# Kernel optimization log

Measured on AMD Instinct MI355X. Metric: run time of the kernel, lower is better.

The kernel has to match this reference:

```python
import jax, jax.numpy as jnp
import numpy as np

NUM_HEADS = 16
DIM_HEAD = 64
SCALE = DIM_HEAD ** -0.5


def setup_inputs() -> dict:
    key = jax.random.key(0)
    k1, k2, k3 = jax.random.split(key, 3)
    b, s, h = 2, 2048, 1024
    x = jax.random.normal(k1, (b, s, h), dtype=jnp.float32)
    w_qkv = jax.random.normal(k2, (3 * h, h), dtype=jnp.float32) * (h ** -0.5)
    w_out = jax.random.normal(k3, (h, h), dtype=jnp.float32) * (h ** -0.5)
    b_out = jnp.zeros((h,), dtype=jnp.float32)
    return {"x": x, "w_qkv": w_qkv, "w_out": w_out, "b_out": b_out}


def reference(x, w_qkv, w_out, b_out):
    b, s, hid = x.shape
    # qkv projection (no bias): [b, s, 3*hid]
    qkv = jnp.einsum('bsh,oh->bso', x, w_qkv)
    # split order in original rearrange is (qkv, heads, dim_head)
    qkv = qkv.reshape(b, s, 3, NUM_HEADS, DIM_HEAD)
    q = jnp.transpose(qkv[:, :, 0], (0, 2, 1, 3))  # [b, H, s, d]
    k = jnp.transpose(qkv[:, :, 1], (0, 2, 1, 3))
    v = jnp.transpose(qkv[:, :, 2], (0, 2, 1, 3))
    # naive attention: full [b, H, s, s] score matrix, as in the source
    att = jnp.einsum('bhxd,bhyd->bhxy', q, k) * SCALE
    att = jax.nn.softmax(att, axis=-1)
    out = jnp.einsum('bhxy,bhyd->bhxd', att, v)  # [b, H, s, d]
    out = jnp.transpose(out, (0, 2, 1, 3)).reshape(b, s, NUM_HEADS * DIM_HEAD)
    return jnp.einsum('bsi,oi->bso', out, w_out) + b_out
```

## Files before the change

### kernel.cpp

```cpp
#include <hip/hip_runtime.h>
#include <hip/hip_bf16.h>

#define B_ 2
#define S_ 2048
#define HID 1024
#define NH 16
#define DH 64
#define QKV_N (3*HID)
#define M_ROWS (B_*S_)

typedef __attribute__((ext_vector_type(8))) short short8;
typedef __attribute__((ext_vector_type(4))) short short4v;
typedef __attribute__((ext_vector_type(4))) float floatx4;
typedef unsigned int uint;

__device__ __forceinline__ short8 load8(const __hip_bfloat16* p) {
    return *(const short8*)p;
}

#if __has_builtin(__builtin_amdgcn_exp2f)
#define EXP2F(x) __builtin_amdgcn_exp2f(x)
#else
#define EXP2F(x) exp2f(x)
#endif

__device__ __forceinline__ uint pack_bf16_2(float lo, float hi) {
    uint ul = __float_as_uint(lo) + 0x8000u;
    uint uh = __float_as_uint(hi) + 0x8000u;
    return __builtin_amdgcn_perm(uh, ul, 0x07060302);
}
__device__ __forceinline__ uint pack_bf16_2_rtne(float lo, float hi) {
    uint ul = __float_as_uint(lo); ul += 0x7FFFu + ((ul >> 16) & 1u);
    uint uh = __float_as_uint(hi); uh += 0x7FFFu + ((uh >> 16) & 1u);
    return __builtin_amdgcn_perm(uh, ul, 0x07060302);
}

#define ASYNC16(gptr, lptr) \
    __builtin_amdgcn_global_load_lds((const __attribute__((address_space(1))) void*)(gptr), \
                                     (__attribute__((address_space(3))) void*)(lptr), 16, 0, 0)

__global__ __launch_bounds__(256) void cvt_all(
    const float* __restrict__ x, const float* __restrict__ wq,
    const float* __restrict__ wo, __hip_bfloat16* __restrict__ out)
{
    const int n0 = M_ROWS * HID, n1 = QKV_N * HID;
    int i = (blockIdx.x * 256 + threadIdx.x) * 4;
    const float* src; int off;
    if (i < n0)           { src = x;  off = i; }
    else if (i < n0 + n1) { src = wq; off = i - n0; }
    else                  { src = wo; off = i - n0 - n1; }
    float4 v = *(const float4*)(src + off);
    uint2 r;
    r.x = pack_bf16_2_rtne(v.x, v.y);
    r.y = pack_bf16_2_rtne(v.z, v.w);
    *(uint2*)(out + i) = r;
}

#define BK 64
template<int MODE>
__global__ __launch_bounds__(256) void gemm_bt_kernel(
    const __hip_bfloat16* __restrict__ A,
    const __hip_bfloat16* __restrict__ Bw,
    const float* __restrict__ biasf,
    __hip_bfloat16* __restrict__ C,
    float* __restrict__ Cf,
    __hip_bfloat16* __restrict__ VT,
    int Mdim, int Ndim, int Kdim)
{
    __shared__ alignas(16) __hip_bfloat16 As[2][128 * BK];
    __shared__ alignas(16) __hip_bfloat16 Bs[2][128 * BK];

    const int tid  = threadIdx.x;
    const int wave = tid >> 6;
    const int lane = tid & 63;
    const int q = lane >> 4;
    const int r = lane & 15;
    const int m_blk = blockIdx.y * 128;
    const int n_blk = blockIdx.x * 128;
    const int wm = (wave >> 1) * 64;
    const int wn = (wave & 1) * 64;

    const int srow = tid >> 3;
    const int cglob = (tid & 7) ^ ((tid >> 3) & 7);
    const __hip_bfloat16* gA = A + (size_t)(m_blk + srow) * Kdim + cglob * 8;
    const __hip_bfloat16* gB = Bw + (size_t)(n_blk + srow) * Kdim + cglob * 8;
    const int ldso = tid * 8;

    floatx4 acc[4][4];
#pragma unroll
    for (int i = 0; i < 4; i++)
#pragma unroll
        for (int j = 0; j < 4; j++) acc[i][j] = (floatx4){0.f, 0.f, 0.f, 0.f};

    const int niter = Kdim / BK;
#pragma unroll
    for (int c = 0; c < 4; c++) {
        ASYNC16(gA + (size_t)(c * 32) * Kdim, &As[0][ldso + c * 2048]);
        ASYNC16(gB + (size_t)(c * 32) * Kdim, &Bs[0][ldso + c * 2048]);
    }
    __builtin_amdgcn_s_waitcnt(0x0F70);
    __syncthreads();

    for (int it = 0; it < niter; it++) {
        const int cur = it & 1, nxt = cur ^ 1;
        if (it + 1 < niter) {
            const int kt = (it + 1) * BK;
#pragma unroll
            for (int c = 0; c < 4; c++) {
                ASYNC16(gA + kt + (size_t)(c * 32) * Kdim, &As[nxt][ldso + c * 2048]);
                ASYNC16(gB + kt + (size_t)(c * 32) * Kdim, &Bs[nxt][ldso + c * 2048]);
            }
        }
#pragma unroll
        for (int kh = 0; kh < 2; kh++) {
            short8 a[4], b[4];
#pragma unroll
            for (int i = 0; i < 4; i++)
                a[i] = *(const short8*)&As[cur][(wm + i * 16 + r) * BK + (((kh * 4 + q) ^ (r & 7)) * 8)];
#pragma unroll
            for (int j = 0; j < 4; j++)
                b[j] = *(const short8*)&Bs[cur][(wn + j * 16 + r) * BK + (((kh * 4 + q) ^ (r & 7)) * 8)];
#pragma unroll
            for (int i = 0; i < 4; i++)
#pragma unroll
                for (int j = 0; j < 4; j++)
                    acc[i][j] = __builtin_amdgcn_mfma_f32_16x16x32_bf16(a[i], b[j], acc[i][j], 0, 0, 0);
        }
        __builtin_amdgcn_s_waitcnt(0x0F70);
        __syncthreads();
    }

#pragma unroll
    for (int i = 0; i < 4; i++) {
#pragma unroll
        for (int j = 0; j < 4; j++) {
#pragma unroll
            for (int reg = 0; reg < 4; reg++) {
                int m = m_blk + wm + i * 16 + q * 4 + reg;
                int n = n_blk + wn + j * 16 + r;
                float v = acc[i][j][reg];
                if (MODE == 2) {
                    Cf[(size_t)m * Ndim + n] = v + biasf[n];
                } else {
                    __hip_bfloat16 hv = __float2bfloat16(v);
                    if (n < 2 * HID) {
                        C[(size_t)m * QKV_N + n] = hv;
                    } else {
                        int dfull = n - 2 * HID;
                        int bidx = m >> 11;
                        int s = m & (S_ - 1);
                        int c = s & 63;
                        int sp = (s & ~63) | ((c & 15) << 2) | ((c >> 4) & 3);
                        VT[((size_t)bidx * HID + dfull) * S_ + sp] = hv;
                    }
                }
            }
        }
    }
}

#define KT 64
#define PPAD 72
#define SCALE2 0.18033688f
#define FM2 23.083120f

__global__ __launch_bounds__(256, 2) void flash_kernel(
    const __hip_bfloat16* __restrict__ qkv,
    const __hip_bfloat16* __restrict__ VTp,
    __hip_bfloat16* __restrict__ O)
{
    __shared__ alignas(16) __hip_bfloat16 lds_k[2][64 * 64];
    __shared__ alignas(16) __hip_bfloat16 lds_v[2][64 * 64];
    __shared__ alignas(16) __hip_bfloat16 lds_p[4][32 * PPAD];

    const int tid  = threadIdx.x;
    const int wave = tid >> 6;
    const int lane = tid & 63;
    const int q = lane >> 4;
    const int r = lane & 15;
    const int bh = blockIdx.x;
    const int b  = bh >> 4;
    const int h  = bh & 15;
    const int s0 = blockIdx.y * 128 + wave * 32;

    const __hip_bfloat16* Qbase = qkv + (size_t)b * S_ * QKV_N + h * DH;
    const __hip_bfloat16* Kbase = Qbase + HID;
    const __hip_bfloat16* Vbase = VTp + ((size_t)b * HID + h * DH) * S_;

    const int sr = wave * 16 + (lane >> 3);
    const int cglob = (lane & 7) ^ ((lane >> 3) & 7);
    const __hip_bfloat16* gK = Kbase + (size_t)sr * QKV_N + cglob * 8;
    const __hip_bfloat16* gV = Vbase + (size_t)sr * S_ + cglob * 8;
    const int ldso = sr * 64 + (lane & 7) * 8;

    short8 a_q[2][2];
#pragma unroll
    for (int rt = 0; rt < 2; rt++)
#pragma unroll
        for (int kh = 0; kh < 2; kh++)
            a_q[rt][kh] = load8(Qbase + (size_t)(s0 + rt * 16 + r) * QKV_N + kh * 32 + q * 8);

    floatx4 o_acc[2][4];
    floatx4 l_acc[2];
#pragma unroll
    for (int rt = 0; rt < 2; rt++) {
        l_acc[rt] = (floatx4){0.f, 0.f, 0.f, 0.f};
#pragma unroll
        for (int nb = 0; nb < 4; nb++) o_acc[rt][nb] = (floatx4){0.f, 0.f, 0.f, 0.f};
    }

    short8 ones;
#pragma unroll
    for (int i = 0; i < 8; i++) ones[i] = (short)0x3F80;

    __hip_bfloat16* Pw = &lds_p[wave][0];

#pragma unroll
    for (int c = 0; c < 2; c++) {
        ASYNC16(gK + (size_t)(c * 8) * QKV_N, &lds_k[0][ldso + c * 512]);
        ASYNC16(gV + (size_t)(c * 8) * S_,    &lds_v[0][ldso + c * 512]);
    }
    __builtin_amdgcn_s_waitcnt(0x0F70);
    __syncthreads();

    for (int it = 0; it < S_ / KT; it++) {
        const int cur = it & 1, nxt = cur ^ 1;
        if (it + 1 < S_ / KT) {
            const int ktn = (it + 1) * KT;
#pragma unroll
            for (int c = 0; c < 2; c++) {
                ASYNC16(gK + (size_t)(ktn + c * 8) * QKV_N, &lds_k[nxt][ldso + c * 512]);
                ASYNC16(gV + (size_t)(c * 8) * S_ + ktn,    &lds_v[nxt][ldso + c * 512]);
            }
        }

        short8 bk[4][2];
#pragma unroll
        for (int ct = 0; ct < 4; ct++)
#pragma unroll
            for (int kh = 0; kh < 2; kh++)
                bk[ct][kh] = *(const short8*)&lds_k[cur][(ct * 16 + r) * 64 + ((kh * 4 + q) ^ (r & 7)) * 8];

#pragma unroll
        for (int rt = 0; rt < 2; rt++) {
            floatx4 sc[4];
#pragma unroll
            for (int ct = 0; ct < 4; ct++) {
                floatx4 z = (floatx4){0.f, 0.f, 0.f, 0.f};
                z = __builtin_amdgcn_mfma_f32_16x16x32_bf16(a_q[rt][0], bk[ct][0], z, 0, 0, 0);
                z = __builtin_amdgcn_mfma_f32_16x16x32_bf16(a_q[rt][1], bk[ct][1], z, 0, 0, 0);
                sc[ct] = z;
            }
#pragma unroll
            for (int reg = 0; reg < 4; reg++) {
                float e0 = EXP2F(fmaf(sc[0][reg], SCALE2, -FM2));
                float e1 = EXP2F(fmaf(sc[1][reg], SCALE2, -FM2));
                float e2 = EXP2F(fmaf(sc[2][reg], SCALE2, -FM2));
                float e3 = EXP2F(fmaf(sc[3][reg], SCALE2, -FM2));
                uint2 pw;
                pw.x = pack_bf16_2(e0, e1);
                pw.y = pack_bf16_2(e2, e3);
                *(uint2*)&Pw[(rt * 16 + q * 4 + reg) * PPAD + 4 * r] = pw;
            }
        }
        __builtin_amdgcn_s_waitcnt(0xc07f);

        short8 vb[4][2];
#pragma unroll
        for (int nb = 0; nb < 4; nb++)
#pragma unroll
            for (int kh = 0; kh < 2; kh++)
                vb[nb][kh] = *(const short8*)&lds_v[cur][(nb * 16 + r) * 64 + ((kh * 4 + q) ^ (r & 7)) * 8];

#pragma unroll
        for (int rt = 0; rt < 2; rt++) {
            short8 pa0 = *(const short8*)&Pw[(rt * 16 + r) * PPAD + q * 8];
            short8 pa1 = *(const short8*)&Pw[(rt * 16 + r) * PPAD + 32 + q * 8];
            l_acc[rt] = __builtin_amdgcn_mfma_f32_16x16x32_bf16(pa0, ones, l_acc[rt], 0, 0, 0);
            l_acc[rt] = __builtin_amdgcn_mfma_f32_16x16x32_bf16(pa1, ones, l_acc[rt], 0, 0, 0);
#pragma unroll
            for (int nb = 0; nb < 4; nb++) {
                o_acc[rt][nb] = __builtin_amdgcn_mfma_f32_16x16x32_bf16(pa0, vb[nb][0], o_acc[rt][nb], 0, 0, 0);
                o_acc[rt][nb] = __builtin_amdgcn_mfma_f32_16x16x32_bf16(pa1, vb[nb][1], o_acc[rt][nb], 0, 0, 0);
            }
        }
        __builtin_amdgcn_s_waitcnt(0x0F70);
        __syncthreads();
    }

#pragma unroll
    for (int rt = 0; rt < 2; rt++) {
#pragma unroll
        for (int reg = 0; reg < 4; reg++) {
            float inv = 1.f / l_acc[rt][reg];
            int srow2 = s0 + rt * 16 + q * 4 + reg;
            __hip_bfloat16* Orow = O + ((size_t)b * S_ + srow2) * HID + h * DH;
#pragma unroll
            for (int nb = 0; nb < 4; nb++)
                Orow[nb * 16 + r] = __float2bfloat16(o_acc[rt][nb][reg] * inv);
        }
    }
}

extern "C" void kernel_launch(void* const* d_in, const int* in_sizes, int n_in,
                              void* d_out, int out_size, void* d_ws, size_t ws_size,
                              hipStream_t stream) {
    const float* x_f     = (const float*)d_in[0];
    const float* w_qkv_f = (const float*)d_in[1];
    const float* w_out_f = (const float*)d_in[2];
    const float* b_out_f = (const float*)d_in[3];
    float* out = (float*)d_out;

    __hip_bfloat16* xb      = (__hip_bfloat16*)d_ws;
    __hip_bfloat16* wqkvb   = xb    + (size_t)M_ROWS * HID;
    __hip_bfloat16* woutb   = wqkvb + (size_t)QKV_N * HID;
    __hip_bfloat16* qkv_ws  = woutb + (size_t)HID * HID;
    __hip_bfloat16* vt_ws   = qkv_ws + (size_t)M_ROWS * QKV_N;
    __hip_bfloat16* attn_ws = vt_ws + (size_t)B_ * HID * S_;

    dim3 blk(256);
    {
        int ntot = M_ROWS * HID + QKV_N * HID + HID * HID;
        cvt_all<<<dim3(ntot / 1024), blk, 0, stream>>>(x_f, w_qkv_f, w_out_f, xb);
    }

    gemm_bt_kernel<1><<<dim3(QKV_N / 128, M_ROWS / 128), blk, 0, stream>>>(
        xb, wqkvb, nullptr, qkv_ws, nullptr, vt_ws, M_ROWS, QKV_N, HID);
    flash_kernel<<<dim3(B_ * NH, S_ / 128), dim3(256), 0, stream>>>(qkv_ws, vt_ws, attn_ws);
    gemm_bt_kernel<2><<<dim3(HID / 128, M_ROWS / 128), blk, 0, stream>>>(
        attn_ws, woutb, b_out_f, nullptr, out, nullptr, M_ROWS, HID, HID);
}
```

Baseline: 203.6 us.

## Triple-buffer GEMM and flash-attention loads with single barrier per iteration

Both the GEMM and flash kernels move from double-buffered async global-to-LDS loads to a three-stage ring buffer. Each iteration now uses a partial vmcnt wait and a raw s_barrier, replacing the full drain plus __syncthreads, so two tiles stay in flight while one is computed. The GEMM also drops to BK=32 with unswizzled LDS layout, gains an M-tile template parameter with occupancy hints, and the output projection uses 64-row tiles to launch more blocks. The costs are more LDS per block and possible bank conflicts from removing the XOR swizzle in the GEMM.

```diff
diff --git a/kernel.cpp b/kernel.cpp
--- a/kernel.cpp
+++ b/kernel.cpp
@@ -38,6 +38,7 @@
 #define ASYNC16(gptr, lptr) \
     __builtin_amdgcn_global_load_lds((const __attribute__((address_space(1))) void*)(gptr), \
                                      (__attribute__((address_space(3))) void*)(lptr), 16, 0, 0)
+#define RAW_BARRIER() asm volatile("s_barrier" ::: "memory")
 
 __global__ __launch_bounds__(256) void cvt_all(
     const float* __restrict__ x, const float* __restrict__ wq,
@@ -56,9 +57,10 @@
     *(uint2*)(out + i) = r;
 }
 
-#define BK 64
-template<int MODE>
-__global__ __launch_bounds__(256) void gemm_bt_kernel(
+#define BK 32
+#define NITER 32
+template<int MODE, int TMB>
+__global__ __launch_bounds__(256, (TMB == 128) ? 3 : 4) void gemm_bt_kernel(
     const __hip_bfloat16* __restrict__ A,
     const __hip_bfloat16* __restrict__ Bw,
     const float* __restrict__ biasf,
@@ -67,71 +69,73 @@
     __hip_bfloat16* __restrict__ VT,
     int Mdim, int Ndim, int Kdim)
 {
-    __shared__ alignas(16) __hip_bfloat16 As[2][128 * BK];
-    __shared__ alignas(16) __hip_bfloat16 Bs[2][128 * BK];
+    constexpr int NI = TMB / 32;
+    constexpr int CA = TMB / 64;
+    constexpr int WAITG = 0x0F70 | (CA + 2);
+    __shared__ alignas(16) __hip_bfloat16 As[3][TMB * BK];
+    __shared__ alignas(16) __hip_bfloat16 Bs[3][128 * BK];
 
     const int tid  = threadIdx.x;
     const int wave = tid >> 6;
     const int lane = tid & 63;
     const int q = lane >> 4;
     const int r = lane & 15;
-    const int m_blk = blockIdx.y * 128;
+    const int m_blk = blockIdx.y * TMB;
     const int n_blk = blockIdx.x * 128;
-    const int wm = (wave >> 1) * 64;
+    const int wm = (wave >> 1) * (TMB / 2);
     const int wn = (wave & 1) * 64;
 
-    const int srow = tid >> 3;
-    const int cglob = (tid & 7) ^ ((tid >> 3) & 7);
-    const __hip_bfloat16* gA = A + (size_t)(m_blk + srow) * Kdim + cglob * 8;
-    const __hip_bfloat16* gB = Bw + (size_t)(n_blk + srow) * Kdim + cglob * 8;
-    const int ldso = tid * 8;
-
-    floatx4 acc[4][4];
-#pragma unroll
-    for (int i = 0; i < 4; i++)
+    const __hip_bfloat16* Abase = A + (size_t)m_blk * Kdim;
+    const __hip_bfloat16* Bbase = Bw + (size_t)n_blk * Kdim;
+
+    floatx4 acc[NI][4];
+#pragma unroll
+    for (int i = 0; i < NI; i++)
 #pragma unroll
         for (int j = 0; j < 4; j++) acc[i][j] = (floatx4){0.f, 0.f, 0.f, 0.f};
 
-    const int niter = Kdim / BK;
-#pragma unroll
-    for (int c = 0; c < 4; c++) {
-        ASYNC16(gA + (size_t)(c * 32) * Kdim, &As[0][ldso + c * 2048]);
-        ASYNC16(gB + (size_t)(c * 32) * Kdim, &Bs[0][ldso + c * 2048]);
-    }
+    auto stage = [&](int bf, int kt) {
+#pragma unroll
+        for (int c = 0; c < CA; c++) {
+            int ch = tid + c * 256;
+            ASYNC16(Abase + (size_t)(ch >> 2) * Kdim + kt + (ch & 3) * 8, &As[bf][ch * 8]);
+        }
+#pragma unroll
+        for (int c = 0; c < 2; c++) {
+            int ch = tid + c * 256;
+            ASYNC16(Bbase + (size_t)(ch >> 2) * Kdim + kt + (ch & 3) * 8, &Bs[bf][ch * 8]);
+        }
+    };
+    auto compute = [&](int bf) {
+        short8 a[NI], b[4];
+#pragma unroll
+        for (int i = 0; i < NI; i++) a[i] = *(const short8*)&As[bf][(wm + i * 16 + r) * BK + q * 8];
+#pragma unroll
+        for (int j = 0; j < 4; j++) b[j] = *(const short8*)&Bs[bf][(wn + j * 16 + r) * BK + q * 8];
+#pragma unroll
+        for (int i = 0; i < NI; i++)
+#pragma unroll
+            for (int j = 0; j < 4; j++)
+                acc[i][j] = __builtin_amdgcn_mfma_f32_16x16x32_bf16(a[i], b[j], acc[i][j], 0, 0, 0);
+    };
+
+    stage(0, 0);
+    stage(1, BK);
+    for (int it = 0; it < NITER - 2; it++) {
+        __builtin_amdgcn_s_waitcnt(WAITG);
+        RAW_BARRIER();
+        stage((it + 2) % 3, (it + 2) * BK);
+        compute(it % 3);
+    }
+    __builtin_amdgcn_s_waitcnt(WAITG);
+    RAW_BARRIER();
+    compute((NITER - 2) % 3);
     __builtin_amdgcn_s_waitcnt(0x0F70);
-    __syncthreads();
-
-    for (int it = 0; it < niter; it++) {
-        const int cur = it & 1, nxt = cur ^ 1;
-        if (it + 1 < niter) {
-            const int kt = (it + 1) * BK;
-#pragma unroll
-            for (int c = 0; c < 4; c++) {
-                ASYNC16(gA + kt + (size_t)(c * 32) * Kdim, &As[nxt][ldso + c * 2048]);
-                ASYNC16(gB + kt + (size_t)(c * 32) * Kdim, &Bs[nxt][ldso + c * 2048]);
-            }
-        }
-#pragma unroll
-        for (int kh = 0; kh < 2; kh++) {
-            short8 a[4], b[4];
-#pragma unroll
-            for (int i = 0; i < 4; i++)
-                a[i] = *(const short8*)&As[cur][(wm + i * 16 + r) * BK + (((kh * 4 + q) ^ (r & 7)) * 8)];
-#pragma unroll
-            for (int j = 0; j < 4; j++)
-                b[j] = *(const short8*)&Bs[cur][(wn + j * 16 + r) * BK + (((kh * 4 + q) ^ (r & 7)) * 8)];
-#pragma unroll
-            for (int i = 0; i < 4; i++)
-#pragma unroll
-                for (int j = 0; j < 4; j++)
-                    acc[i][j] = __builtin_amdgcn_mfma_f32_16x16x32_bf16(a[i], b[j], acc[i][j], 0, 0, 0);
-        }
-        __builtin_amdgcn_s_waitcnt(0x0F70);
-        __syncthreads();
-    }
-
-#pragma unroll
-    for (int i = 0; i < 4; i++) {
+    RAW_BARRIER();
+    compute((NITER - 1) % 3);
+
+#pragma unroll
+    for (int i = 0; i < NI; i++) {
 #pragma unroll
         for (int j = 0; j < 4; j++) {
 #pragma unroll
@@ -169,8 +173,8 @@
     const __hip_bfloat16* __restrict__ VTp,
     __hip_bfloat16* __restrict__ O)
 {
-    __shared__ alignas(16) __hip_bfloat16 lds_k[2][64 * 64];
-    __shared__ alignas(16) __hip_bfloat16 lds_v[2][64 * 64];
+    __shared__ alignas(16) __hip_bfloat16 lds_k[3][64 * 64];
+    __shared__ alignas(16) __hip_bfloat16 lds_v[3][64 * 64];
     __shared__ alignas(16) __hip_bfloat16 lds_p[4][32 * PPAD];
 
     const int tid  = threadIdx.x;
@@ -193,13 +197,6 @@
     const __hip_bfloat16* gV = Vbase + (size_t)sr * S_ + cglob * 8;
     const int ldso = sr * 64 + (lane & 7) * 8;
 
-    short8 a_q[2][2];
-#pragma unroll
-    for (int rt = 0; rt < 2; rt++)
-#pragma unroll
-        for (int kh = 0; kh < 2; kh++)
-            a_q[rt][kh] = load8(Qbase + (size_t)(s0 + rt * 16 + r) * QKV_N + kh * 32 + q * 8);
-
     floatx4 o_acc[2][4];
     floatx4 l_acc[2];
 #pragma unroll
@@ -215,32 +212,22 @@
 
     __hip_bfloat16* Pw = &lds_p[wave][0];
 
-#pragma unroll
-    for (int c = 0; c < 2; c++) {
-        ASYNC16(gK + (size_t)(c * 8) * QKV_N, &lds_k[0][ldso + c * 512]);
-        ASYNC16(gV + (size_t)(c * 8) * S_,    &lds_v[0][ldso + c * 512]);
-    }
-    __builtin_amdgcn_s_waitcnt(0x0F70);
-    __syncthreads();
-
-    for (int it = 0; it < S_ / KT; it++) {
-        const int cur = it & 1, nxt = cur ^ 1;
-        if (it + 1 < S_ / KT) {
-            const int ktn = (it + 1) * KT;
-#pragma unroll
-            for (int c = 0; c < 2; c++) {
-                ASYNC16(gK + (size_t)(ktn + c * 8) * QKV_N, &lds_k[nxt][ldso + c * 512]);
-                ASYNC16(gV + (size_t)(c * 8) * S_ + ktn,    &lds_v[nxt][ldso + c * 512]);
-            }
-        }
-
+    auto stage = [&](int bf, int kt) {
+#pragma unroll
+        for (int c = 0; c < 2; c++) {
+            ASYNC16(gK + (size_t)(kt + c * 8) * QKV_N, &lds_k[bf][ldso + c * 512]);
+            ASYNC16(gV + (size_t)(c * 8) * S_ + kt,    &lds_v[bf][ldso + c * 512]);
+        }
+    };
+
+    short8 a_q[2][2];
+    auto compute = [&](int bf) {
         short8 bk[4][2];
 #pragma unroll
         for (int ct = 0; ct < 4; ct++)
 #pragma unroll
             for (int kh = 0; kh < 2; kh++)
-                bk[ct][kh] = *(const short8*)&lds_k[cur][(ct * 16 + r) * 64 + ((kh * 4 + q) ^ (r & 7)) * 8];
-
+                bk[ct][kh] = *(const short8*)&lds_k[bf][(ct * 16 + r) * 64 + ((kh * 4 + q) ^ (r & 7)) * 8];
 #pragma unroll
         for (int rt = 0; rt < 2; rt++) {
             floatx4 sc[4];
@@ -270,8 +257,7 @@
         for (int nb = 0; nb < 4; nb++)
 #pragma unroll
             for (int kh = 0; kh < 2; kh++)
-                vb[nb][kh] = *(const short8*)&lds_v[cur][(nb * 16 + r) * 64 + ((kh * 4 + q) ^ (r & 7)) * 8];
-
+                vb[nb][kh] = *(const short8*)&lds_v[bf][(nb * 16 + r) * 64 + ((kh * 4 + q) ^ (r & 7)) * 8];
 #pragma unroll
         for (int rt = 0; rt < 2; rt++) {
             short8 pa0 = *(const short8*)&Pw[(rt * 16 + r) * PPAD + q * 8];
@@ -284,9 +270,29 @@
                 o_acc[rt][nb] = __builtin_amdgcn_mfma_f32_16x16x32_bf16(pa1, vb[nb][1], o_acc[rt][nb], 0, 0, 0);
             }
         }
-        __builtin_amdgcn_s_waitcnt(0x0F70);
-        __syncthreads();
-    }
+    };
+
+    stage(0, 0);
+#pragma unroll
+    for (int rt = 0; rt < 2; rt++)
+#pragma unroll
+        for (int kh = 0; kh < 2; kh++)
+            a_q[rt][kh] = load8(Qbase + (size_t)(s0 + rt * 16 + r) * QKV_N + kh * 32 + q * 8);
+    __builtin_amdgcn_s_waitcnt(0x0F70);
+    stage(1, KT);
+
+    for (int it = 0; it < 30; it++) {
+        __builtin_amdgcn_s_waitcnt(0x0F74);
+        RAW_BARRIER();
+        stage((it + 2) % 3, (it + 2) * KT);
+        compute(it % 3);
+    }
+    __builtin_amdgcn_s_waitcnt(0x0F74);
+    RAW_BARRIER();
+    compute(0);
+    __builtin_amdgcn_s_waitcnt(0x0F70);
+    RAW_BARRIER();
+    compute(1);
 
 #pragma unroll
     for (int rt = 0; rt < 2; rt++) {
@@ -324,9 +330,9 @@
         cvt_all<<<dim3(ntot / 1024), blk, 0, stream>>>(x_f, w_qkv_f, w_out_f, xb);
     }
 
-    gemm_bt_kernel<1><<<dim3(QKV_N / 128, M_ROWS / 128), blk, 0, stream>>>(
+    gemm_bt_kernel<1, 128><<<dim3(QKV_N / 128, M_ROWS / 128), blk, 0, stream>>>(
         xb, wqkvb, nullptr, qkv_ws, nullptr, vt_ws, M_ROWS, QKV_N, HID);
     flash_kernel<<<dim3(B_ * NH, S_ / 128), dim3(256), 0, stream>>>(qkv_ws, vt_ws, attn_ws);
-    gemm_bt_kernel<2><<<dim3(HID / 128, M_ROWS / 128), blk, 0, stream>>>(
+    gemm_bt_kernel<2, 64><<<dim3(HID / 128, M_ROWS / 64), blk, 0, stream>>>(
         attn_ws, woutb, b_out_f, nullptr, out, nullptr, M_ROWS, HID, HID);
 }
```

Measured after the change: 193.3 us. 1.05x faster.
